# Performance work log

Hardware: AMD Instinct MI355X
Metric: run time of the kernel (lower is better)

The kernel has to match this reference:

```python
import jax, jax.numpy as jnp
import numpy as np

N = 100_000   # nodes
E = 2_400_000 # edges (before self-loops)
H = 32        # hidden_size == num_features
NEG_SLOPE = 0.2


def setup_inputs() -> dict:
    key = jax.random.key(0)
    ks = jax.random.split(key, 16)
    rn = lambda k, s, sc=1.0: (jax.random.normal(k, s, dtype=jnp.float32) * sc)
    return {
        'x': rn(ks[0], (N, H)),
        'edge_index': jax.random.randint(ks[1], (2, E), 0, N, dtype=jnp.int32),
        'conv_W': rn(ks[2], (H, H), 0.1),
        'conv_att_src': rn(ks[3], (H,), 0.1),
        'conv_att_dst': rn(ks[4], (H,), 0.1),
        'conv_bias': jnp.zeros((H,), jnp.float32),
        'gru_Wih0': rn(ks[5], (3 * H, H), 0.1),
        'gru_Whh0': rn(ks[6], (3 * H, H), 0.1),
        'gru_bih0': rn(ks[7], (3 * H,), 0.1),
        'gru_bhh0': rn(ks[8], (3 * H,), 0.1),
        'gru_Wih1': rn(ks[9], (3 * H, H), 0.1),
        'gru_Whh1': rn(ks[10], (3 * H, H), 0.1),
        'gru_bih1': rn(ks[11], (3 * H,), 0.1),
        'gru_bhh1': rn(ks[12], (3 * H,), 0.1),
        'lin_W': rn(ks[13], (1, H), 0.1),
        'lin_b': jnp.zeros((1,), jnp.float32),
    }


def _gat_conv(x, edge_index, W, att_src, att_dst, bias):
    # PyG GATConv, heads=1, concat=True, add_self_loops=True.
    h = x @ W.T                                     # [N, H]
    loop = jnp.arange(N, dtype=edge_index.dtype)
    src = jnp.concatenate([edge_index[0], loop])    # [E+N]
    dst = jnp.concatenate([edge_index[1], loop])
    a_s = h @ att_src                               # [N]
    a_d = h @ att_dst
    e = jax.nn.leaky_relu(a_s[src] + a_d[dst], NEG_SLOPE)  # [E+N]
    # segment softmax over incoming edges of each dst node
    m = jax.ops.segment_max(e, dst, num_segments=N)        # each node has a self-loop
    p = jnp.exp(e - m[dst])
    denom = jax.ops.segment_sum(p, dst, num_segments=N)
    alpha = p / denom[dst]                                  # [E+N]
    out = jax.ops.segment_sum(alpha[:, None] * h[src], dst, num_segments=N)
    return out + bias


def _gru_cell_zero_h(x, Wih, Whh, bih, bhh):
    # Single GRU step with h_prev = 0 (seq_len == 1, h0 zeros). Gate order: r, z, n.
    gi = x @ Wih.T + bih                    # [N, 3H]
    h0 = jnp.zeros_like(x)
    gh = h0 @ Whh.T + bhh                   # [N, 3H] (Whh contributes zero)
    i_r, i_z, i_n = jnp.split(gi, 3, axis=-1)
    h_r, h_z, h_n = jnp.split(gh, 3, axis=-1)
    r = jax.nn.sigmoid(i_r + h_r)
    z = jax.nn.sigmoid(i_z + h_z)
    n = jnp.tanh(i_n + r * h_n)
    return (1.0 - z) * n                    # + z * h0, h0 = 0


def reference(x, edge_index, conv_W, conv_att_src, conv_att_dst, conv_bias,
              gru_Wih0, gru_Whh0, gru_bih0, gru_bhh0,
              gru_Wih1, gru_Whh1, gru_bih1, gru_bhh1,
              lin_W, lin_b):
    h = jax.nn.relu(x)
    h = _gat_conv(h, edge_index, conv_W, conv_att_src, conv_att_dst, conv_bias)
    h = _gru_cell_zero_h(h, gru_Wih0, gru_Whh0, gru_bih0, gru_bhh0)
    h = _gru_cell_zero_h(h, gru_Wih1, gru_Whh1, gru_bih1, gru_bhh1)
    h = _gat_conv(h, edge_index, conv_W, conv_att_src, conv_att_dst, conv_bias)
    return h @ lin_W.T + lin_b              # [N, 1]
```

## Files before the change

### kernel.cpp

```cpp
#include <hip/hip_runtime.h>
#include <hip/hip_fp16.h>
#include <math.h>

#define Hd 32
#define NEG 0.2f
#define BSH 8
#define BN (1 << BSH)
#define CHUNK 4096
#define NBUCK_MAX 512
#define WP 36

__device__ __forceinline__ float lrelu(float x) { return x > 0.f ? x : NEG * x; }
__device__ __forceinline__ float fsigm(float x) { return 1.f / (1.f + __expf(-x)); }
__device__ __forceinline__ float ftanh(float x) { return 1.f - 2.f / (__expf(2.f * x) + 1.f); }


__global__ void k_histb(const int* __restrict__ dst, int* __restrict__ counts,
                        int E, int nchunk, int nbuck)
{
    __shared__ int hh[NBUCK_MAX];
    int c = blockIdx.x, t = threadIdx.x;
    for (int i = t; i < nbuck; i += 256) hh[i] = 0;
    __syncthreads();
    int beg = c * CHUNK, end = min(beg + CHUNK, E);
    for (int k = beg + t; k < end; k += 256) atomicAdd(&hh[dst[k] >> BSH], 1);
    __syncthreads();
    for (int i = t; i < nbuck; i += 256) counts[i * nchunk + c] = hh[i];
}

__global__ void k_scan1(const int* __restrict__ in, int* __restrict__ bsum, int L)
{
    __shared__ int sd[256];
    int t = threadIdx.x;
    int i = blockIdx.x * 256 + t;
    sd[t] = (i < L) ? in[i] : 0;
    __syncthreads();
    for (int s = 128; s > 0; s >>= 1) {
        if (t < s) sd[t] += sd[t + s];
        __syncthreads();
    }
    if (t == 0) bsum[blockIdx.x] = sd[0];
}

__global__ void k_scan2(int* __restrict__ bsum, int nb)
{
    __shared__ int sd[1024];
    int t = threadIdx.x;
    int v = (t < nb) ? bsum[t] : 0;
    sd[t] = v;
    __syncthreads();
    for (int o = 1; o < 1024; o <<= 1) {
        int x = (t >= o) ? sd[t - o] : 0;
        __syncthreads();
        sd[t] += x;
        __syncthreads();
    }
    if (t < nb) bsum[t] = sd[t] - v;
}

__global__ void k_scan3(const int* __restrict__ in, const int* __restrict__ bsum,
                        int* __restrict__ out, int L)
{
    __shared__ int sd[256];
    int t = threadIdx.x;
    int i = blockIdx.x * 256 + t;
    int v = (i < L) ? in[i] : 0;
    sd[t] = v;
    __syncthreads();
    for (int o = 1; o < 256; o <<= 1) {
        int x = (t >= o) ? sd[t - o] : 0;
        __syncthreads();
        sd[t] += x;
        __syncthreads();
    }
    if (i < L) out[i] = bsum[blockIdx.x] + sd[t] - v;
}

__global__ void k_scatterb(const int* __restrict__ src, const int* __restrict__ dst,
                           const int* __restrict__ counts, const int* __restrict__ cstart,
                           unsigned* __restrict__ tmp, int E, int nchunk, int nbuck)
{
    __shared__ unsigned long long ebuf[CHUNK];
    __shared__ int lstart[NBUCK_MAX];
    __shared__ int gbase[NBUCK_MAX];
    __shared__ int cur[NBUCK_MAX];
    __shared__ int lscan[256];
    int c = blockIdx.x, t = threadIdx.x;
    int b0 = 2 * t, b1 = b0 + 1;
    int n0 = (b0 < nbuck) ? counts[(size_t)b0 * nchunk + c] : 0;
    int n1 = (b1 < nbuck) ? counts[(size_t)b1 * nchunk + c] : 0;
    if (b0 < nbuck) gbase[b0] = cstart[(size_t)b0 * nchunk + c];
    if (b1 < nbuck) gbase[b1] = cstart[(size_t)b1 * nchunk + c];
    int pair = n0 + n1;
    lscan[t] = pair;
    __syncthreads();
    for (int o = 1; o < 256; o <<= 1) {
        int x = (t >= o) ? lscan[t - o] : 0;
        __syncthreads();
        lscan[t] += x;
        __syncthreads();
    }
    int excl = lscan[t] - pair;
    if (b0 < nbuck) { lstart[b0] = excl;      cur[b0] = excl; }
    if (b1 < nbuck) { lstart[b1] = excl + n0; cur[b1] = excl + n0; }
    __syncthreads();
    int beg = c * CHUNK, end = min(beg + CHUNK, E);
    for (int k = beg + t; k < end; k += 256) {
        int d = dst[k];
        int pos = atomicAdd(&cur[d >> BSH], 1);
        ebuf[pos] = ((unsigned long long)(unsigned)d << 17) | (unsigned)src[k];
    }
    __syncthreads();
    int csize = end - beg;
    for (int i = t; i < csize; i += 256) {
        unsigned long long v = ebuf[i];
        int d = (int)(v >> 17);
        int b = d >> BSH;
        tmp[gbase[b] + (i - lstart[b])] =
            ((unsigned)(d & (BN - 1)) << 17) | (unsigned)(v & 0x1FFFFu);
    }
}

__global__ void k_place2(const unsigned* __restrict__ tmp, const int* __restrict__ cstart,
                         int* __restrict__ csr, int* __restrict__ off_g, int* __restrict__ cnt_g,
                         int N, int E, int nchunk, int nbuck)
{
    __shared__ int lcnt[BN];
    __shared__ int lscan[BN];
    __shared__ int lcur[BN];
    int b = blockIdx.x, t = threadIdx.x;
    int bstart = cstart[(size_t)b * nchunk];
    int bend = (b + 1 < nbuck) ? cstart[(size_t)(b + 1) * nchunk] : E;
    lcnt[t] = 0;
    __syncthreads();
    for (int k = bstart + t; k < bend; k += 256)
        atomicAdd(&lcnt[tmp[k] >> 17], 1);
    __syncthreads();
    int c = lcnt[t];
    lscan[t] = c;
    __syncthreads();
    for (int o = 1; o < 256; o <<= 1) {
        int x = (t >= o) ? lscan[t - o] : 0;
        __syncthreads();
        lscan[t] += x;
        __syncthreads();
    }
    int o0 = bstart + lscan[t] - c;
    int node = (b << BSH) + t;
    lcur[t] = o0;
    if (node < N) { off_g[node] = o0; cnt_g[node] = c; }
    __syncthreads();
    for (int k = bstart + t; k < bend; k += 256) {
        unsigned v = tmp[k];
        int pos = atomicAdd(&lcur[v >> 17], 1);
        csr[pos] = (int)(v & 0x1FFFFu);
    }
}


template<bool RELU>
__global__ void k_node_proj(const float* __restrict__ x, const float* __restrict__ W,
                            const float* __restrict__ att_s, const float* __restrict__ att_d,
                            __half* __restrict__ h16, float* __restrict__ as_, float* __restrict__ ad_,
                            int N)
{
    __shared__ float Wl[Hd][Hd + 1];
    __shared__ float xr[8][Hd];
    int tid = threadIdx.x;
    for (int i = tid; i < Hd * Hd; i += 256) Wl[i >> 5][i & 31] = W[i];
    int li = tid >> 5, j = tid & 31;
    float asj = att_s[j], adj = att_d[j];
    __syncthreads();
#pragma unroll 1
    for (int tile = 0; tile < 4; tile++) {
        int node = (blockIdx.x * 4 + tile) * 8 + li;
        float v = 0.f;
        if (node < N) v = x[(size_t)node * Hd + j];
        if (RELU) v = fmaxf(v, 0.f);
        xr[li][j] = v;
        float a = 0.f;
#pragma unroll
        for (int k = 0; k < Hd; k++) a += xr[li][k] * Wl[j][k];
        float s = a * asj, d = a * adj;
#pragma unroll
        for (int m = 16; m > 0; m >>= 1) { s += __shfl_xor(s, m, 32); d += __shfl_xor(d, m, 32); }
        if (node < N) {
            h16[(size_t)node * Hd + j] = __float2half(a);
            if (j == 0) { as_[node] = s; ad_[node] = d; }
        }
    }
}

template<int MODE>
__global__ void k_gather(const __half* __restrict__ h16, const float* __restrict__ as_,
                         const float* __restrict__ ad_, const int* __restrict__ cnt,
                         const int* __restrict__ off, const int* __restrict__ csr_src,
                         const float* __restrict__ bias, const float* __restrict__ linW,
                         const float* __restrict__ linb, float* __restrict__ out, int N)
{
    int idx = blockIdx.x * 256 + threadIdx.x;
    int n = idx >> 5;
    if (n >= N) return;
    int j = threadIdx.x & 31;
    int sg = j >> 3, q = j & 7;
    int beg = off[n], deg = cnt[n];
    float adn = ad_[n];

    float denp = 0.f;
    float4 acc = make_float4(0.f, 0.f, 0.f, 0.f);

    for (int c = 0; c < deg; c += 32) {
        int k = c + j;
        int sj = n; float pj = 0.f;
        if (k < deg) { sj = csr_src[beg + k]; pj = __expf(lrelu(as_[sj] + adn)); }
        denp += pj;
#pragma unroll
        for (int t = 0; t < 8; t++) {
            float p = __shfl(pj, t, 8);
            int   s = __shfl(sj, t, 8);
            uint2 rv = ((const uint2*)(h16 + (size_t)s * Hd))[q];
            float2 f01 = __half22float2(*reinterpret_cast<const __half2*>(&rv.x));
            float2 f23 = __half22float2(*reinterpret_cast<const __half2*>(&rv.y));
            acc.x = fmaf(p, f01.x, acc.x);
            acc.y = fmaf(p, f01.y, acc.y);
            acc.z = fmaf(p, f23.x, acc.z);
            acc.w = fmaf(p, f23.y, acc.w);
        }
    }

    float pself = __expf(lrelu(as_[n] + adn));
    if (sg == 0) {
        uint2 rv = ((const uint2*)(h16 + (size_t)n * Hd))[q];
        float2 f01 = __half22float2(*reinterpret_cast<const __half2*>(&rv.x));
        float2 f23 = __half22float2(*reinterpret_cast<const __half2*>(&rv.y));
        acc.x = fmaf(pself, f01.x, acc.x);
        acc.y = fmaf(pself, f01.y, acc.y);
        acc.z = fmaf(pself, f23.x, acc.z);
        acc.w = fmaf(pself, f23.y, acc.w);
    }
#pragma unroll
    for (int o = 16; o > 0; o >>= 1) denp += __shfl_xor(denp, o, 32);
    float den = denp + pself;
#pragma unroll
    for (int o = 8; o <= 16; o <<= 1) {
        acc.x += __shfl_xor(acc.x, o, 32);
        acc.y += __shfl_xor(acc.y, o, 32);
        acc.z += __shfl_xor(acc.z, o, 32);
        acc.w += __shfl_xor(acc.w, o, 32);
    }
    float inv = 1.f / den;
    float4 b4 = ((const float4*)bias)[q];
    if (MODE == 0) {
        if (sg == 0) {
            float4 o4;
            o4.x = fmaf(acc.x, inv, b4.x);
            o4.y = fmaf(acc.y, inv, b4.y);
            o4.z = fmaf(acc.z, inv, b4.z);
            o4.w = fmaf(acc.w, inv, b4.w);
            ((float4*)(out + (size_t)n * Hd))[q] = o4;
        }
    } else {
        float4 w4 = ((const float4*)linW)[q];
        float s = fmaf(acc.x, inv, b4.x) * w4.x
                + fmaf(acc.y, inv, b4.y) * w4.y
                + fmaf(acc.z, inv, b4.z) * w4.z
                + fmaf(acc.w, inv, b4.w) * w4.w;
#pragma unroll
        for (int o = 1; o <= 4; o <<= 1) s += __shfl_xor(s, o, 32);
        if (j == 0) out[n] = s + linb[0];
    }
}

__global__ __launch_bounds__(256) void k_gru2(
    const float* __restrict__ in,
    const float* __restrict__ Wih0, const float* __restrict__ bih0, const float* __restrict__ bhh0,
    const float* __restrict__ Wih1, const float* __restrict__ bih1, const float* __restrict__ bhh1,
    float* __restrict__ out, int N)
{
    __shared__ __align__(16) float W0l[96 * WP];
    __shared__ __align__(16) float W1l[96 * WP];
    __shared__ __align__(16) float rows[8][4][Hd];
    int tid = threadIdx.x;
    for (int i = tid; i < 96 * Hd; i += 256) {
        int r = i >> 5, k = i & 31;
        W0l[r * WP + k] = Wih0[i];
        W1l[r * WP + k] = Wih1[i];
    }
    int g = tid >> 5, j = tid & 31;
    int node0 = blockIdx.x * 32 + g * 4;
#pragma unroll
    for (int i = 0; i < 4; i++) {
        int node = node0 + i;
        rows[g][i][j] = (node < N) ? in[(size_t)node * Hd + j] : 0.f;
    }
    float br0 = bih0[j], bz0 = bih0[32 + j], bn0 = bih0[64 + j];
    float hr0 = bhh0[j], hz0 = bhh0[32 + j], hn0 = bhh0[64 + j];
    float br1 = bih1[j], bz1 = bih1[32 + j], bn1 = bih1[64 + j];
    float hr1 = bhh1[j], hz1 = bhh1[32 + j], hn1 = bhh1[64 + j];
    __syncthreads();

    float ar[4], az[4], an[4];
#pragma unroll
    for (int i = 0; i < 4; i++) { ar[i] = br0; az[i] = bz0; an[i] = bn0; }
#pragma unroll 2
    for (int k4 = 0; k4 < 8; k4++) {
        float4 wr = *(const float4*)&W0l[(j     ) * WP + k4 * 4];
        float4 wz = *(const float4*)&W0l[(32 + j) * WP + k4 * 4];
        float4 wn = *(const float4*)&W0l[(64 + j) * WP + k4 * 4];
#pragma unroll
        for (int i = 0; i < 4; i++) {
            float4 xv = *(const float4*)&rows[g][i][k4 * 4];
            ar[i] = fmaf(xv.x, wr.x, ar[i]); ar[i] = fmaf(xv.y, wr.y, ar[i]);
            ar[i] = fmaf(xv.z, wr.z, ar[i]); ar[i] = fmaf(xv.w, wr.w, ar[i]);
            az[i] = fmaf(xv.x, wz.x, az[i]); az[i] = fmaf(xv.y, wz.y, az[i]);
            az[i] = fmaf(xv.z, wz.z, az[i]); az[i] = fmaf(xv.w, wz.w, az[i]);
            an[i] = fmaf(xv.x, wn.x, an[i]); an[i] = fmaf(xv.y, wn.y, an[i]);
            an[i] = fmaf(xv.z, wn.z, an[i]); an[i] = fmaf(xv.w, wn.w, an[i]);
        }
    }
#pragma unroll
    for (int i = 0; i < 4; i++) {
        float r = fsigm(ar[i] + hr0);
        float z = fsigm(az[i] + hz0);
        float t = ftanh(an[i] + r * hn0);
        rows[g][i][j] = (1.f - z) * t;
    }

#pragma unroll
    for (int i = 0; i < 4; i++) { ar[i] = br1; az[i] = bz1; an[i] = bn1; }
#pragma unroll 2
    for (int k4 = 0; k4 < 8; k4++) {
        float4 wr = *(const float4*)&W1l[(j     ) * WP + k4 * 4];
        float4 wz = *(const float4*)&W1l[(32 + j) * WP + k4 * 4];
        float4 wn = *(const float4*)&W1l[(64 + j) * WP + k4 * 4];
#pragma unroll
        for (int i = 0; i < 4; i++) {
            float4 xv = *(const float4*)&rows[g][i][k4 * 4];
            ar[i] = fmaf(xv.x, wr.x, ar[i]); ar[i] = fmaf(xv.y, wr.y, ar[i]);
            ar[i] = fmaf(xv.z, wr.z, ar[i]); ar[i] = fmaf(xv.w, wr.w, ar[i]);
            az[i] = fmaf(xv.x, wz.x, az[i]); az[i] = fmaf(xv.y, wz.y, az[i]);
            az[i] = fmaf(xv.z, wz.z, az[i]); az[i] = fmaf(xv.w, wz.w, az[i]);
            an[i] = fmaf(xv.x, wn.x, an[i]); an[i] = fmaf(xv.y, wn.y, an[i]);
            an[i] = fmaf(xv.z, wn.z, an[i]); an[i] = fmaf(xv.w, wn.w, an[i]);
        }
    }
#pragma unroll
    for (int i = 0; i < 4; i++) {
        float r = fsigm(ar[i] + hr1);
        float z = fsigm(az[i] + hz1);
        float t = ftanh(an[i] + r * hn1);
        int node = node0 + i;
        if (node < N) out[(size_t)node * Hd + j] = (1.f - z) * t;
    }
}

extern "C" void kernel_launch(void* const* d_in, const int* in_sizes, int n_in,
                              void* d_out, int out_size, void* d_ws, size_t ws_size,
                              hipStream_t stream)
{
    const float* x    = (const float*)d_in[0];
    const int*   ei   = (const int*)d_in[1];
    const float* W    = (const float*)d_in[2];
    const float* atts = (const float*)d_in[3];
    const float* attd = (const float*)d_in[4];
    const float* bias = (const float*)d_in[5];
    const float* Wih0 = (const float*)d_in[6];
    const float* bih0 = (const float*)d_in[8];
    const float* bhh0 = (const float*)d_in[9];
    const float* Wih1 = (const float*)d_in[10];
    const float* bih1 = (const float*)d_in[12];
    const float* bhh1 = (const float*)d_in[13];
    const float* linW = (const float*)d_in[14];
    const float* linb = (const float*)d_in[15];

    int N = in_sizes[0] / Hd;
    int E = in_sizes[1] / 2;
    const int* src = ei;
    const int* dst = ei + E;
    int nbuck = (N + BN - 1) >> BSH;
    int nchunk = (E + CHUNK - 1) / CHUNK;
    int L = nbuck * nchunk;
    int nbL = (L + 255) / 256;

    __half* h16  = (__half*)d_ws;
    float* base  = (float*)d_ws;
    float* gat   = base + (size_t)N * Hd;
    float* h2    = gat  + (size_t)N * Hd;
    float* as_   = h2   + (size_t)N * Hd;
    float* ad_   = as_ + N;
    int*   cnt   = (int*)(ad_ + N);
    int*   off   = cnt + N;
    int*   counts= off + N;
    int*   cstart= counts + L;
    int*   bsum  = cstart + L;
    int*   csr   = bsum + 1024;
    unsigned* tmp = (unsigned*)gat;

    dim3 blk(256);
    dim3 g_proj((N + 31) / 32);
    dim3 g_nf((N * Hd + 255) / 256);
    dim3 g_gru((N + 31) / 32);

    hipLaunchKernelGGL(k_histb, dim3(nchunk), blk, 0, stream, dst, counts, E, nchunk, nbuck);
    hipLaunchKernelGGL(k_scan1, dim3(nbL), blk, 0, stream, counts, bsum, L);
    hipLaunchKernelGGL(k_scan2, dim3(1), dim3(1024), 0, stream, bsum, nbL);
    hipLaunchKernelGGL(k_scan3, dim3(nbL), blk, 0, stream, counts, bsum, cstart, L);
    hipLaunchKernelGGL(k_scatterb, dim3(nchunk), blk, 0, stream, src, dst, counts, cstart, tmp, E, nchunk, nbuck);
    hipLaunchKernelGGL(k_place2, dim3(nbuck), blk, 0, stream, tmp, cstart, csr, off, cnt, N, E, nchunk, nbuck);

    hipLaunchKernelGGL((k_node_proj<true>), g_proj, blk, 0, stream, x, W, atts, attd, h16, as_, ad_, N);
    hipLaunchKernelGGL((k_gather<0>), g_nf, blk, 0, stream, h16, as_, ad_, cnt, off, csr, bias, linW, linb, gat, N);
    hipLaunchKernelGGL(k_gru2, g_gru, blk, 0, stream, gat, Wih0, bih0, bhh0, Wih1, bih1, bhh1, h2, N);

    hipLaunchKernelGGL((k_node_proj<false>), g_proj, blk, 0, stream, h2, W, atts, attd, h16, as_, ad_, N);
    hipLaunchKernelGGL((k_gather<1>), g_nf, blk, 0, stream, h16, as_, ad_, cnt, off, csr, bias, linW, linb, (float*)d_out, N);
}
```

Before: 203.1 us.

## Fold final linear layer into second GAT projection to gather scalars

Because the output linear layer is linear, it is pushed through the second GAT aggregation: each node's projected feature is reduced to a scalar h·linW together with its source attention score, stored as a float2. The second gather then fetches one float2 per edge instead of a 32-wide half-precision row, and the wide feature write in the second projection is dropped. This cuts the edge-side memory traffic of the last layer, with the bias contribution added separately and rounding that differs slightly from the reference.

```diff
diff --git a/kernel.cpp b/kernel.cpp
--- a/kernel.cpp
+++ b/kernel.cpp
@@ -191,12 +191,45 @@
     }
 }
 
-template<int MODE>
+__global__ void k_node_proj_lin(const float* __restrict__ x, const float* __restrict__ W,
+                                const float* __restrict__ att_s, const float* __restrict__ att_d,
+                                const float* __restrict__ linW,
+                                float2* __restrict__ sv, float* __restrict__ ad_, int N)
+{
+    __shared__ float Wl[Hd][Hd + 1];
+    __shared__ float xr[8][Hd];
+    int tid = threadIdx.x;
+    for (int i = tid; i < Hd * Hd; i += 256) Wl[i >> 5][i & 31] = W[i];
+    int li = tid >> 5, j = tid & 31;
+    float asj = att_s[j], adj = att_d[j], lwj = linW[j];
+    __syncthreads();
+#pragma unroll 1
+    for (int tile = 0; tile < 4; tile++) {
+        int node = (blockIdx.x * 4 + tile) * 8 + li;
+        float v = 0.f;
+        if (node < N) v = x[(size_t)node * Hd + j];
+        xr[li][j] = v;
+        float a = 0.f;
+#pragma unroll
+        for (int k = 0; k < Hd; k++) a += xr[li][k] * Wl[j][k];
+        float s = a * asj, d = a * adj, w = a * lwj;
+#pragma unroll
+        for (int m = 16; m > 0; m >>= 1) {
+            s += __shfl_xor(s, m, 32);
+            d += __shfl_xor(d, m, 32);
+            w += __shfl_xor(w, m, 32);
+        }
+        if (node < N && j == 0) {
+            sv[node] = make_float2(s, w);
+            ad_[node] = d;
+        }
+    }
+}
+
 __global__ void k_gather(const __half* __restrict__ h16, const float* __restrict__ as_,
                          const float* __restrict__ ad_, const int* __restrict__ cnt,
                          const int* __restrict__ off, const int* __restrict__ csr_src,
-                         const float* __restrict__ bias, const float* __restrict__ linW,
-                         const float* __restrict__ linb, float* __restrict__ out, int N)
+                         const float* __restrict__ bias, float* __restrict__ out, int N)
 {
     int idx = blockIdx.x * 256 + threadIdx.x;
     int n = idx >> 5;
@@ -248,27 +281,51 @@
         acc.z += __shfl_xor(acc.z, o, 32);
         acc.w += __shfl_xor(acc.w, o, 32);
     }
-    float inv = 1.f / den;
-    float4 b4 = ((const float4*)bias)[q];
-    if (MODE == 0) {
-        if (sg == 0) {
-            float4 o4;
-            o4.x = fmaf(acc.x, inv, b4.x);
-            o4.y = fmaf(acc.y, inv, b4.y);
-            o4.z = fmaf(acc.z, inv, b4.z);
-            o4.w = fmaf(acc.w, inv, b4.w);
-            ((float4*)(out + (size_t)n * Hd))[q] = o4;
-        }
-    } else {
-        float4 w4 = ((const float4*)linW)[q];
-        float s = fmaf(acc.x, inv, b4.x) * w4.x
-                + fmaf(acc.y, inv, b4.y) * w4.y
-                + fmaf(acc.z, inv, b4.z) * w4.z
-                + fmaf(acc.w, inv, b4.w) * w4.w;
-#pragma unroll
-        for (int o = 1; o <= 4; o <<= 1) s += __shfl_xor(s, o, 32);
-        if (j == 0) out[n] = s + linb[0];
-    }
+    if (sg == 0) {
+        float inv = 1.f / den;
+        float4 b4 = ((const float4*)bias)[q];
+        float4 o4;
+        o4.x = fmaf(acc.x, inv, b4.x);
+        o4.y = fmaf(acc.y, inv, b4.y);
+        o4.z = fmaf(acc.z, inv, b4.z);
+        o4.w = fmaf(acc.w, inv, b4.w);
+        ((float4*)(out + (size_t)n * Hd))[q] = o4;
+    }
+}
+
+__global__ void k_gather_lin(const float2* __restrict__ sv, const float* __restrict__ ad_,
+                             const int* __restrict__ cnt, const int* __restrict__ off,
+                             const int* __restrict__ csr_src,
+                             const float* __restrict__ bias, const float* __restrict__ linW,
+                             const float* __restrict__ linb, float* __restrict__ out, int N)
+{
+    int idx = blockIdx.x * 256 + threadIdx.x;
+    int n = idx >> 5;
+    if (n >= N) return;
+    int j = threadIdx.x & 31;
+    int beg = off[n], deg = cnt[n];
+    float adn = ad_[n];
+
+    float den = 0.f, acc = 0.f;
+    for (int k = beg + j; k < beg + deg; k += 32) {
+        int s = csr_src[k];
+        float2 e = sv[s];
+        float p = __expf(lrelu(e.x + adn));
+        den += p;
+        acc = fmaf(p, e.y, acc);
+    }
+    float bpart = bias[j] * linW[j];
+#pragma unroll
+    for (int o = 16; o > 0; o >>= 1) {
+        den += __shfl_xor(den, o, 32);
+        acc += __shfl_xor(acc, o, 32);
+        bpart += __shfl_xor(bpart, o, 32);
+    }
+    float2 en = sv[n];
+    float pself = __expf(lrelu(en.x + adn));
+    den += pself;
+    acc = fmaf(pself, en.y, acc);
+    if (j == 0) out[n] = acc / den + bpart + linb[0];
 }
 
 __global__ __launch_bounds__(256) void k_gru2(
@@ -388,7 +445,8 @@
     float* h2    = gat  + (size_t)N * Hd;
     float* as_   = h2   + (size_t)N * Hd;
     float* ad_   = as_ + N;
-    int*   cnt   = (int*)(ad_ + N);
+    float2* sv   = (float2*)(ad_ + N);
+    int*   cnt   = (int*)(sv + N);
     int*   off   = cnt + N;
     int*   counts= off + N;
     int*   cstart= counts + L;
@@ -409,9 +467,9 @@
     hipLaunchKernelGGL(k_place2, dim3(nbuck), blk, 0, stream, tmp, cstart, csr, off, cnt, N, E, nchunk, nbuck);
 
     hipLaunchKernelGGL((k_node_proj<true>), g_proj, blk, 0, stream, x, W, atts, attd, h16, as_, ad_, N);
-    hipLaunchKernelGGL((k_gather<0>), g_nf, blk, 0, stream, h16, as_, ad_, cnt, off, csr, bias, linW, linb, gat, N);
+    hipLaunchKernelGGL(k_gather, g_nf, blk, 0, stream, h16, as_, ad_, cnt, off, csr, bias, gat, N);
     hipLaunchKernelGGL(k_gru2, g_gru, blk, 0, stream, gat, Wih0, bih0, bhh0, Wih1, bih1, bhh1, h2, N);
 
-    hipLaunchKernelGGL((k_node_proj<false>), g_proj, blk, 0, stream, h2, W, atts, attd, h16, as_, ad_, N);
-    hipLaunchKernelGGL((k_gather<1>), g_nf, blk, 0, stream, h16, as_, ad_, cnt, off, csr, bias, linW, linb, (float*)d_out, N);
-}
+    hipLaunchKernelGGL(k_node_proj_lin, g_proj, blk, 0, stream, h2, W, atts, attd, linW, sv, ad_, N);
+    hipLaunchKernelGGL(k_gather_lin, g_nf, blk, 0, stream, sv, ad_, cnt, off, csr, bias, linW, linb, (float*)d_out, N);
+}
```

Result: faster. 184.5 us (-9.1%).
